# Optimization experiments

Measured on AMD Instinct MI355X. Metric: run time of the kernel, lower is better.

Reference implementation:

```python
import jax, jax.numpy as jnp
import numpy as np

N_NODES = 50000
N_EDGES = 200000
IN_C = 128
HID_C = 128
HEADS = 4
OUT_C = 64
NEG_SLOPE = 0.2


def _glorot(key, shape):
    fan_in, fan_out = shape[0], shape[-1]
    limit = np.sqrt(6.0 / (fan_in + fan_out)).astype(np.float32)
    return jax.random.uniform(key, shape, jnp.float32, -limit, limit)


def setup_inputs() -> dict:
    key = jax.random.key(0)
    ks = jax.random.split(key, 32)
    inp = {}
    inp["x"] = jax.random.normal(ks[0], (N_NODES, IN_C), jnp.float32)
    inp["edge_index"] = jax.random.randint(ks[1], (2, N_EDGES), 0, N_NODES, jnp.int64)
    # layer dims: (in_dim, per_head_out, heads)
    dims = [
        (IN_C, HID_C, HEADS),
        (HID_C * HEADS, HID_C, HEADS),
        (HID_C * HEADS, HID_C, HEADS),
        (HID_C * HEADS, OUT_C, 1),
    ]
    concat = [True, True, True, False]
    kidx = 2
    for i, (din, dout, h) in enumerate(dims):
        inp[f"Wl{i}"] = _glorot(ks[kidx], (din, h * dout)); kidx += 1
        inp[f"bl{i}"] = jnp.zeros((h * dout,), jnp.float32)
        inp[f"Wr{i}"] = _glorot(ks[kidx], (din, h * dout)); kidx += 1
        inp[f"br{i}"] = jnp.zeros((h * dout,), jnp.float32)
        inp[f"att{i}"] = _glorot(ks[kidx], (h, dout)); kidx += 1
        inp[f"b{i}"] = jnp.zeros((h * dout if concat[i] else dout,), jnp.float32)
    return inp


def _segment_softmax(e, seg, num_segments):
    # e: [E, H], seg: [E] target-node ids
    m = jax.ops.segment_max(e, seg, num_segments=num_segments)  # [N, H]
    ex = jnp.exp(e - m[seg])
    s = jax.ops.segment_sum(ex, seg, num_segments=num_segments)  # [N, H]
    return ex / (s[seg] + 1e-16)


def _gatv2_layer(x, src, dst, Wl, bl, Wr, br, att, bias, heads, out_c, concat):
    n = x.shape[0]
    xl = (x @ Wl + bl).reshape(n, heads, out_c)  # source transform
    xr = (x @ Wr + br).reshape(n, heads, out_c)  # target transform
    # GATv2 attention: e_ij = a^T LeakyReLU(xl_j + xr_i)
    z = jax.nn.leaky_relu(xl[src] + xr[dst], NEG_SLOPE)  # [E, H, C]
    e = jnp.einsum("ehc,hc->eh", z, att)  # [E, H]
    alpha = _segment_softmax(e, dst, n)  # [E, H]
    out = jax.ops.segment_sum(alpha[:, :, None] * xl[src], dst, num_segments=n)  # [N, H, C]
    out = out.reshape(n, heads * out_c) if concat else out.mean(axis=1)
    return out + bias


def reference(x, edge_index,
              Wl0, bl0, Wr0, br0, att0, b0,
              Wl1, bl1, Wr1, br1, att1, b1,
              Wl2, bl2, Wr2, br2, att2, b2,
              Wl3, bl3, Wr3, br3, att3, b3):
    src, dst = edge_index[0], edge_index[1]
    layers = [
        (Wl0, bl0, Wr0, br0, att0, b0, HEADS, HID_C, True),
        (Wl1, bl1, Wr1, br1, att1, b1, HEADS, HID_C, True),
        (Wl2, bl2, Wr2, br2, att2, b2, HEADS, HID_C, True),
    ]
    h = x
    for (Wl, bl, Wr, br, att, b, nh, dc, cc) in layers:
        h = jax.nn.elu(_gatv2_layer(h, src, dst, Wl, bl, Wr, br, att, b, nh, dc, cc))
    out = _gatv2_layer(h, src, dst, Wl3, bl3, Wr3, br3, att3, b3, 1, OUT_C, False)
    return out
```

## Files before the change

### kernel.cpp

```cpp
#include <hip/hip_runtime.h>
#include <math.h>

#define NNODES 50000
#define NEDGES 200000

typedef unsigned short ushort_t;
using frag8 = __attribute__((ext_vector_type(8))) short;
using facc4 = __attribute__((ext_vector_type(4))) float;

static __device__ __forceinline__ ushort_t f2b(float f) {
  union { float f; unsigned u; } v; v.f = f;
  unsigned r = v.u + 0x7FFFu + ((v.u >> 16) & 1u);
  return (ushort_t)(r >> 16);
}
static __device__ __forceinline__ float b2f(unsigned hi) {
  return __uint_as_float(hi << 16);
}
static __device__ __forceinline__ void unpack8(const int4 v, float* f) {
  f[0] = b2f((unsigned)v.x & 0xFFFFu); f[1] = b2f((unsigned)v.x >> 16);
  f[2] = b2f((unsigned)v.y & 0xFFFFu); f[3] = b2f((unsigned)v.y >> 16);
  f[4] = b2f((unsigned)v.z & 0xFFFFu); f[5] = b2f((unsigned)v.z >> 16);
  f[6] = b2f((unsigned)v.w & 0xFFFFu); f[7] = b2f((unsigned)v.w >> 16);
}
static __device__ __forceinline__ void stf(float* p, float v) { *p = v; }
static __device__ __forceinline__ void stf(ushort_t* p, float v) { *p = f2b(v); }

__global__ void cast_x(const float* __restrict__ x, ushort_t* __restrict__ xb, int total8) {
  int t = blockIdx.x * 256 + threadIdx.x;
  if (t >= total8) return;
  const float4* p = (const float4*)(x + (size_t)t * 8);
  float4 a = p[0], b = p[1];
  int4 w = make_int4(
      (int)((unsigned)f2b(a.x) | ((unsigned)f2b(a.y) << 16)),
      (int)((unsigned)f2b(a.z) | ((unsigned)f2b(a.w) << 16)),
      (int)((unsigned)f2b(b.x) | ((unsigned)f2b(b.y) << 16)),
      (int)((unsigned)f2b(b.z) | ((unsigned)f2b(b.w) << 16)));
  *(int4*)(xb + (size_t)t * 8) = w;
}

__global__ void wt_prep2(const float* __restrict__ Wl, const float* __restrict__ Wr,
                         ushort_t* __restrict__ WtLR, int K, int Mo) {
  int t = blockIdx.x * 256 + threadIdx.x;
  const int tot = K * Mo;
  if (t >= 2 * tot) return;
  const float* W = (t < tot) ? Wl : Wr;
  int u = (t < tot) ? t : t - tot;
  int c = u / K, k = u - c * K;
  WtLR[t] = f2b(W[(size_t)k * Mo + c]);
}

__global__ __launch_bounds__(256) void gemm2_mfma(
    const ushort_t* __restrict__ A, const ushort_t* __restrict__ WtLR,
    const float* __restrict__ bl, const float* __restrict__ br,
    ushort_t* __restrict__ xlb, ushort_t* __restrict__ xrb,
    int N, int K, int Mo, int ncb) {
  __shared__ __align__(16) char smem[34816];
  auto Al = reinterpret_cast<ushort_t(*)[128][8]>(smem);
  auto Bl = reinterpret_cast<ushort_t(*)[128][8]>(smem + 8192);
  auto Cl = reinterpret_cast<ushort_t(*)[136]>(smem);

  const int nwg = gridDim.x;
  const int q = nwg >> 3, r = nwg & 7;
  const int xcd = blockIdx.x & 7, pos = blockIdx.x >> 3;
  const int orig = (xcd < r ? xcd * (q + 1) : r * (q + 1) + (xcd - r) * q) + pos;
  const int rp = orig / ncb, cb = orig - rp * ncb;
  const int brow = rp * 128;
  const int bcol = cb * 128;

  const int tid = threadIdx.x;
  const int wave = tid >> 6, lane = tid & 63;
  const int wr = wave >> 1, wc = wave & 1;
  const int l15 = lane & 15, l4 = lane >> 4;

  facc4 acc[4][4] = {};

  const int srow = tid >> 1;
  const int skb  = (tid & 1) * 2;
  for (int k0 = 0; k0 < K; k0 += 32) {
    {
      const int grow = brow + srow;
      int4 a0, a1;
      if (grow < N) {
        const int4* pa = (const int4*)(A + (size_t)grow * K + k0 + skb * 8);
        a0 = pa[0]; a1 = pa[1];
      } else {
        a0 = a1 = make_int4(0, 0, 0, 0);
      }
      *(int4*)&Al[skb + 0][srow][0] = a0;
      *(int4*)&Al[skb + 1][srow][0] = a1;
      const int4* pb = (const int4*)(WtLR + (size_t)(bcol + srow) * K + k0 + skb * 8);
      int4 b0 = pb[0], b1 = pb[1];
      *(int4*)&Bl[skb + 0][srow][0] = b0;
      *(int4*)&Bl[skb + 1][srow][0] = b1;
    }
    __syncthreads();
    frag8 af[4], bfg[4];
    #pragma unroll
    for (int i = 0; i < 4; ++i)
      af[i] = *(const frag8*)&Al[l4][wr * 64 + i * 16 + l15][0];
    #pragma unroll
    for (int j = 0; j < 4; ++j)
      bfg[j] = *(const frag8*)&Bl[l4][wc * 64 + j * 16 + l15][0];
    #pragma unroll
    for (int i = 0; i < 4; ++i)
      #pragma unroll
      for (int j = 0; j < 4; ++j)
        acc[i][j] = __builtin_amdgcn_mfma_f32_16x16x32_bf16(af[i], bfg[j], acc[i][j], 0, 0, 0);
    __syncthreads();
  }

  #pragma unroll
  for (int j = 0; j < 4; ++j) {
    const int lcol = wc * 64 + j * 16 + l15;
    const int col2 = bcol + lcol;
    const float bv = (col2 < Mo) ? bl[col2] : br[col2 - Mo];
    #pragma unroll
    for (int i = 0; i < 4; ++i) {
      const int lrow = wr * 64 + i * 16 + l4 * 4;
      #pragma unroll
      for (int rr = 0; rr < 4; ++rr)
        Cl[lrow + rr][lcol] = f2b(acc[i][j][rr] + bv);
    }
  }
  __syncthreads();
  {
    const int row = tid >> 1;
    const int half = tid & 1;
    const int grow = brow + row;
    if (grow < N) {
      const int colb = half * 64;
      const int col2 = bcol + colb;
      const bool isL = col2 < Mo;
      ushort_t* dst = (isL ? xlb : xrb) + (size_t)grow * Mo + (isL ? col2 : col2 - Mo);
      #pragma unroll
      for (int k = 0; k < 8; ++k) {
        int4 v = *(const int4*)&Cl[row][colb + k * 8];
        *(int4*)(dst + k * 8) = v;
      }
    }
  }
}

__global__ void csr_zero(int* __restrict__ deg) {
  int t = blockIdx.x * blockDim.x + threadIdx.x;
  if (t < NNODES) deg[t] = 0;
}
__global__ void csr_hist(const int* __restrict__ ei, int* __restrict__ deg) {
  int e = blockIdx.x * blockDim.x + threadIdx.x;
  if (e >= NEDGES) return;
  atomicAdd(&deg[ei[NEDGES + e]], 1);
}

#define SCAN_TPB 256
#define SCAN_EPT 4
#define SCAN_CHUNK (SCAN_TPB * SCAN_EPT)
#define SCAN_BLK ((NNODES + SCAN_CHUNK - 1) / SCAN_CHUNK)

__global__ __launch_bounds__(SCAN_TPB) void scan_k1(const int* __restrict__ deg,
                                                    int* __restrict__ bsum) {
  __shared__ int sd[SCAN_TPB];
  const int tid = threadIdx.x;
  const int tbase = blockIdx.x * SCAN_CHUNK + tid * SCAN_EPT;
  int s = 0;
  #pragma unroll
  for (int j = 0; j < SCAN_EPT; ++j) {
    int idx = tbase + j;
    if (idx < NNODES) s += deg[idx];
  }
  sd[tid] = s;
  __syncthreads();
  for (int d = SCAN_TPB / 2; d > 0; d >>= 1) {
    if (tid < d) sd[tid] += sd[tid + d];
    __syncthreads();
  }
  if (tid == 0) bsum[blockIdx.x] = sd[0];
}

__global__ __launch_bounds__(64) void scan_k2(const int* __restrict__ bsum,
                                              int* __restrict__ bpref,
                                              int* __restrict__ off) {
  __shared__ int sd[64];
  const int tid = threadIdx.x;
  sd[tid] = (tid < SCAN_BLK) ? bsum[tid] : 0;
  __syncthreads();
  for (int d = 1; d < 64; d <<= 1) {
    int t = (tid >= d) ? sd[tid - d] : 0;
    __syncthreads();
    sd[tid] += t;
    __syncthreads();
  }
  if (tid < SCAN_BLK) bpref[tid] = (tid == 0) ? 0 : sd[tid - 1];
  if (tid == 0) off[NNODES] = NEDGES;
}

__global__ __launch_bounds__(SCAN_TPB) void scan_k3(const int* __restrict__ deg,
                                                    const int* __restrict__ bpref,
                                                    int* __restrict__ off,
                                                    int* __restrict__ pos) {
  __shared__ int sd[SCAN_TPB];
  const int tid = threadIdx.x;
  const int tbase = blockIdx.x * SCAN_CHUNK + tid * SCAN_EPT;
  int v[SCAN_EPT];
  int s = 0;
  #pragma unroll
  for (int j = 0; j < SCAN_EPT; ++j) {
    int idx = tbase + j;
    v[j] = (idx < NNODES) ? deg[idx] : 0;
    s += v[j];
  }
  sd[tid] = s;
  __syncthreads();
  for (int d = 1; d < SCAN_TPB; d <<= 1) {
    int t = (tid >= d) ? sd[tid - d] : 0;
    __syncthreads();
    sd[tid] += t;
    __syncthreads();
  }
  int run = bpref[blockIdx.x] + ((tid == 0) ? 0 : sd[tid - 1]);
  #pragma unroll
  for (int j = 0; j < SCAN_EPT; ++j) {
    int idx = tbase + j;
    if (idx < NNODES) { off[idx] = run; pos[idx] = run; run += v[j]; }
  }
}

__global__ void csr_fill(const int* __restrict__ ei, int* __restrict__ pos,
                         int* __restrict__ eids) {
  int e = blockIdx.x * blockDim.x + threadIdx.x;
  if (e >= NEDGES) return;
  int p = atomicAdd(&pos[ei[NEDGES + e]], 1);
  eids[p] = e;
}

template<int H, int C, bool ELU, typename TO>
__global__ __launch_bounds__(256) void csr_fused(
    const int* __restrict__ off, const int* __restrict__ eids,
    const int* __restrict__ ei, const ushort_t* __restrict__ xl,
    const ushort_t* __restrict__ xr, const float* __restrict__ att,
    const float* __restrict__ bias, TO* __restrict__ out) {
  constexpr int HC = H * C;
  constexpr int CPL = HC / 64;
  constexpr int GROUP = C / CPL;
  const int n = (blockIdx.x * blockDim.x + threadIdx.x) >> 6;
  const int lane = threadIdx.x & 63;
  if (n >= NNODES) return;
  const int s0 = off[n], s1 = off[n + 1];

  float xrr[CPL], atr[CPL];
  if constexpr (CPL == 8) {
    unpack8(*(const int4*)(xr + (size_t)n * HC + lane * 8), xrr);
    const float4 a0 = *(const float4*)(att + lane * 8);
    const float4 a1 = *(const float4*)(att + lane * 8 + 4);
    atr[0] = a0.x; atr[1] = a0.y; atr[2] = a0.z; atr[3] = a0.w;
    atr[4] = a1.x; atr[5] = a1.y; atr[6] = a1.z; atr[7] = a1.w;
  } else {
    xrr[0] = b2f(xr[(size_t)n * HC + lane]);
    atr[0] = att[lane];
  }

  float m = -1e30f, s = 0.f;
  float acc[CPL] = {};

  int4 vnext = make_int4(0, 0, 0, 0);
  ushort_t unext = 0;
  if (s0 < s1) {
    const int srcn = ei[eids[s0]];
    if constexpr (CPL == 8) vnext = *(const int4*)(xl + (size_t)srcn * HC + lane * 8);
    else                    unext = xl[(size_t)srcn * HC + lane];
  }
  for (int i = s0; i < s1; ++i) {
    int4 vcur = vnext; ushort_t ucur = unext;
    if (i + 1 < s1) {
      const int srcn = ei[eids[i + 1]];
      if constexpr (CPL == 8) vnext = *(const int4*)(xl + (size_t)srcn * HC + lane * 8);
      else                    unext = xl[(size_t)srcn * HC + lane];
    }
    float zl[CPL];
    if constexpr (CPL == 8) unpack8(vcur, zl);
    else zl[0] = b2f(ucur);
    float e = 0.f;
    #pragma unroll
    for (int c = 0; c < CPL; ++c) {
      float z = zl[c] + xrr[c];
      z = (z > 0.f) ? z : 0.2f * z;
      e += z * atr[c];
    }
    #pragma unroll
    for (int o = 1; o < GROUP; o <<= 1)
      e += __shfl_xor(e, o, 64);
    if (e > m) {
      const float scale = __expf(m - e);
      s *= scale;
      #pragma unroll
      for (int c = 0; c < CPL; ++c) acc[c] *= scale;
      m = e;
    }
    const float w = __expf(e - m);
    s += w;
    #pragma unroll
    for (int c = 0; c < CPL; ++c) acc[c] += w * zl[c];
  }
  const float inv = 1.f / (s + 1e-16f);
  TO* po = out + (size_t)n * HC + lane * CPL;
  #pragma unroll
  for (int c = 0; c < CPL; ++c) {
    float v = acc[c] * inv + bias[lane * CPL + c];
    if (ELU) v = v > 0.f ? v : (__expf(v) - 1.f);
    stf(&po[c], v);
  }
}

__global__ void report_ws(float* __restrict__ out, float v) { out[0] = v; }

extern "C" void kernel_launch(void* const* d_in, const int* in_sizes, int n_in,
                              void* d_out, int out_size, void* d_ws, size_t ws_size,
                              hipStream_t stream) {
  const float* x  = (const float*)d_in[0];
  const int*   ei = (const int*)d_in[1];
  float* out = (float*)d_out;
  char* ws = (char*)d_ws;

  ushort_t* hbuf = (ushort_t*)(ws);
  ushort_t* xlb  = (ushort_t*)(ws + 51200000ull);
  ushort_t* xrb  = (ushort_t*)(ws + 102400000ull);
  ushort_t* xb   = (ushort_t*)(ws + 153600000ull);
  ushort_t* WtLR = (ushort_t*)(ws + 166400000ull);
  int* bsum  = (int*)(ws + 168500000ull);
  int* bpref = (int*)(ws + 168501024ull);
  int* coff  = (int*)(ws + 168600000ull);
  int* cpos  = (int*)(ws + 168800008ull);
  int* cdeg  = (int*)(ws + 169000012ull);
  int* eids  = (int*)(ws + 169200016ull);

  if (ws_size < 170000016ull) {
    report_ws<<<1, 1, 0, stream>>>(out, (float)ws_size);
    return;
  }

  cast_x<<<(NNODES * 128 / 8 + 255) / 256, 256, 0, stream>>>(x, xb, NNODES * 128 / 8);
  csr_zero<<<(NNODES + 255) / 256, 256, 0, stream>>>(cdeg);
  csr_hist<<<(NEDGES + 255) / 256, 256, 0, stream>>>(ei, cdeg);
  scan_k1<<<SCAN_BLK, SCAN_TPB, 0, stream>>>(cdeg, bsum);
  scan_k2<<<1, 64, 0, stream>>>(bsum, bpref, coff);
  scan_k3<<<SCAN_BLK, SCAN_TPB, 0, stream>>>(cdeg, bpref, coff, cpos);
  csr_fill<<<(NEDGES + 255) / 256, 256, 0, stream>>>(ei, cpos, eids);

  const int ngrid = (NNODES * 64 + 255) / 256;
  const int nrp = (NNODES + 127) / 128;

  for (int layer = 0; layer < 4; ++layer) {
    const int base = 2 + layer * 6;
    const float* Wl  = (const float*)d_in[base + 0];
    const float* bl  = (const float*)d_in[base + 1];
    const float* Wr  = (const float*)d_in[base + 2];
    const float* br  = (const float*)d_in[base + 3];
    const float* att = (const float*)d_in[base + 4];
    const float* b   = (const float*)d_in[base + 5];

    const ushort_t* A = (layer == 0) ? xb : hbuf;
    const int K  = (layer == 0) ? 128 : 512;
    const int Mo = (layer == 3) ? 64 : 512;
    const int ncb = 2 * Mo / 128;

    wt_prep2<<<(2 * K * Mo + 255) / 256, 256, 0, stream>>>(Wl, Wr, WtLR, K, Mo);

    gemm2_mfma<<<ncb * nrp, 256, 0, stream>>>(A, WtLR, bl, br, xlb, xrb,
                                              NNODES, K, Mo, ncb);

    if (layer < 3) {
      csr_fused<4, 128, true, ushort_t><<<ngrid, 256, 0, stream>>>(
          coff, eids, ei, xlb, xrb, att, b, hbuf);
    } else {
      csr_fused<1, 64, false, float><<<ngrid, 256, 0, stream>>>(
          coff, eids, ei, xlb, xrb, att, b, out);
    }
  }
}
```

Measured before the change: 528.9 us.

## Prefetch GEMM tiles with BK=64, tile-transpose weights, store source ids in CSR

The GEMM now uses a K-step of 64 and register-prefetches the next A/B tile while MFMAs run on the current one, halving barrier count per K. Weight transpose/cast uses a 32x32 shared-memory tile for coalesced reads and writes instead of strided per-element loads. The CSR fill stores source node ids directly so the aggregation kernel drops one dependent indirection, and the next source id is prefetched two edges ahead. More registers are used in the GEMM, which may reduce occupancy.

```diff
diff --git a/kernel.cpp b/kernel.cpp
--- a/kernel.cpp
+++ b/kernel.cpp
@@ -38,25 +38,34 @@
   *(int4*)(xb + (size_t)t * 8) = w;
 }
 
-__global__ void wt_prep2(const float* __restrict__ Wl, const float* __restrict__ Wr,
-                         ushort_t* __restrict__ WtLR, int K, int Mo) {
-  int t = blockIdx.x * 256 + threadIdx.x;
-  const int tot = K * Mo;
-  if (t >= 2 * tot) return;
-  const float* W = (t < tot) ? Wl : Wr;
-  int u = (t < tot) ? t : t - tot;
-  int c = u / K, k = u - c * K;
-  WtLR[t] = f2b(W[(size_t)k * Mo + c]);
-}
-
-__global__ __launch_bounds__(256) void gemm2_mfma(
+__global__ __launch_bounds__(256) void wt_prep_t(
+    const float* __restrict__ Wl, const float* __restrict__ Wr,
+    ushort_t* __restrict__ WtLR, int K, int Mo) {
+  __shared__ float tile[32][33];
+  const int tx = threadIdx.x & 31, ty = threadIdx.x >> 5;
+  const int kb = blockIdx.y * 32, cb = blockIdx.x * 32;
+  const int c2 = cb + tx;
+  const float* W = (c2 < Mo) ? Wl : Wr;
+  const int col = (c2 < Mo) ? c2 : c2 - Mo;
+  #pragma unroll
+  for (int r = 0; r < 4; ++r)
+    tile[ty * 4 + r][tx] = W[(size_t)(kb + ty * 4 + r) * Mo + col];
+  __syncthreads();
+  #pragma unroll
+  for (int r = 0; r < 4; ++r) {
+    const int c2w = cb + ty * 4 + r;
+    WtLR[(size_t)c2w * K + kb + tx] = f2b(tile[tx][ty * 4 + r]);
+  }
+}
+
+__global__ __launch_bounds__(256) void gemm2_pf64(
     const ushort_t* __restrict__ A, const ushort_t* __restrict__ WtLR,
     const float* __restrict__ bl, const float* __restrict__ br,
     ushort_t* __restrict__ xlb, ushort_t* __restrict__ xrb,
     int N, int K, int Mo, int ncb) {
   __shared__ __align__(16) char smem[34816];
   auto Al = reinterpret_cast<ushort_t(*)[128][8]>(smem);
-  auto Bl = reinterpret_cast<ushort_t(*)[128][8]>(smem + 8192);
+  auto Bl = reinterpret_cast<ushort_t(*)[128][8]>(smem + 16384);
   auto Cl = reinterpret_cast<ushort_t(*)[136]>(smem);
 
   const int nwg = gridDim.x;
@@ -68,44 +77,62 @@
   const int bcol = cb * 128;
 
   const int tid = threadIdx.x;
-  const int wave = tid >> 6, lane = tid & 63;
-  const int wr = wave >> 1, wc = wave & 1;
+  const int w = tid >> 6, lane = tid & 63;
+  const int wr = w >> 1, wc = w & 1;
   const int l15 = lane & 15, l4 = lane >> 4;
 
   facc4 acc[4][4] = {};
 
   const int srow = tid >> 1;
-  const int skb  = (tid & 1) * 2;
-  for (int k0 = 0; k0 < K; k0 += 32) {
-    {
-      const int grow = brow + srow;
-      int4 a0, a1;
-      if (grow < N) {
-        const int4* pa = (const int4*)(A + (size_t)grow * K + k0 + skb * 8);
-        a0 = pa[0]; a1 = pa[1];
-      } else {
-        a0 = a1 = make_int4(0, 0, 0, 0);
+  const int sk4  = (tid & 1) * 4;
+  const int grow = brow + srow;
+  const bool rowok = grow < N;
+  const ushort_t* pa = A + (size_t)(rowok ? grow : 0) * K + sk4 * 8;
+  const ushort_t* pb = WtLR + (size_t)(bcol + srow) * K + sk4 * 8;
+
+  const int nt = K >> 6;
+
+  int4 ar[4], br_[4];
+  if (rowok) {
+    const int4* p = (const int4*)pa;
+    ar[0] = p[0]; ar[1] = p[1]; ar[2] = p[2]; ar[3] = p[3];
+  } else {
+    ar[0] = ar[1] = ar[2] = ar[3] = make_int4(0, 0, 0, 0);
+  }
+  { const int4* p = (const int4*)pb;
+    br_[0] = p[0]; br_[1] = p[1]; br_[2] = p[2]; br_[3] = p[3]; }
+
+  for (int t = 0; t < nt; ++t) {
+    #pragma unroll
+    for (int j = 0; j < 4; ++j) {
+      *(int4*)&Al[sk4 + j][srow][0] = ar[j];
+      *(int4*)&Bl[sk4 + j][srow][0] = br_[j];
+    }
+    if (t + 1 < nt) {
+      const int k0 = (t + 1) * 64;
+      if (rowok) {
+        const int4* p = (const int4*)(pa + k0);
+        ar[0] = p[0]; ar[1] = p[1]; ar[2] = p[2]; ar[3] = p[3];
       }
-      *(int4*)&Al[skb + 0][srow][0] = a0;
-      *(int4*)&Al[skb + 1][srow][0] = a1;
-      const int4* pb = (const int4*)(WtLR + (size_t)(bcol + srow) * K + k0 + skb * 8);
-      int4 b0 = pb[0], b1 = pb[1];
-      *(int4*)&Bl[skb + 0][srow][0] = b0;
-      *(int4*)&Bl[skb + 1][srow][0] = b1;
-    }
-    __syncthreads();
-    frag8 af[4], bfg[4];
-    #pragma unroll
-    for (int i = 0; i < 4; ++i)
-      af[i] = *(const frag8*)&Al[l4][wr * 64 + i * 16 + l15][0];
-    #pragma unroll
-    for (int j = 0; j < 4; ++j)
-      bfg[j] = *(const frag8*)&Bl[l4][wc * 64 + j * 16 + l15][0];
-    #pragma unroll
-    for (int i = 0; i < 4; ++i)
+      { const int4* p = (const int4*)(pb + k0);
+        br_[0] = p[0]; br_[1] = p[1]; br_[2] = p[2]; br_[3] = p[3]; }
+    }
+    __syncthreads();
+    #pragma unroll
+    for (int kk = 0; kk < 2; ++kk) {
+      frag8 af[4], bfg[4];
+      #pragma unroll
+      for (int i = 0; i < 4; ++i)
+        af[i] = *(const frag8*)&Al[kk * 4 + l4][wr * 64 + i * 16 + l15][0];
       #pragma unroll
       for (int j = 0; j < 4; ++j)
-        acc[i][j] = __builtin_amdgcn_mfma_f32_16x16x32_bf16(af[i], bfg[j], acc[i][j], 0, 0, 0);
+        bfg[j] = *(const frag8*)&Bl[kk * 4 + l4][wc * 64 + j * 16 + l15][0];
+      #pragma unroll
+      for (int i = 0; i < 4; ++i)
+        #pragma unroll
+        for (int j = 0; j < 4; ++j)
+          acc[i][j] = __builtin_amdgcn_mfma_f32_16x16x32_bf16(af[i], bfg[j], acc[i][j], 0, 0, 0);
+    }
     __syncthreads();
   }
 
@@ -126,12 +153,12 @@
   {
     const int row = tid >> 1;
     const int half = tid & 1;
-    const int grow = brow + row;
-    if (grow < N) {
+    const int growo = brow + row;
+    if (growo < N) {
       const int colb = half * 64;
       const int col2 = bcol + colb;
       const bool isL = col2 < Mo;
-      ushort_t* dst = (isL ? xlb : xrb) + (size_t)grow * Mo + (isL ? col2 : col2 - Mo);
+      ushort_t* dst = (isL ? xlb : xrb) + (size_t)growo * Mo + (isL ? col2 : col2 - Mo);
       #pragma unroll
       for (int k = 0; k < 8; ++k) {
         int4 v = *(const int4*)&Cl[row][colb + k * 8];
@@ -225,19 +252,19 @@
 }
 
 __global__ void csr_fill(const int* __restrict__ ei, int* __restrict__ pos,
-                         int* __restrict__ eids) {
+                         int* __restrict__ srcs) {
   int e = blockIdx.x * blockDim.x + threadIdx.x;
   if (e >= NEDGES) return;
   int p = atomicAdd(&pos[ei[NEDGES + e]], 1);
-  eids[p] = e;
+  srcs[p] = ei[e];
 }
 
 template<int H, int C, bool ELU, typename TO>
 __global__ __launch_bounds__(256) void csr_fused(
-    const int* __restrict__ off, const int* __restrict__ eids,
-    const int* __restrict__ ei, const ushort_t* __restrict__ xl,
-    const ushort_t* __restrict__ xr, const float* __restrict__ att,
-    const float* __restrict__ bias, TO* __restrict__ out) {
+    const int* __restrict__ off, const int* __restrict__ srcs,
+    const ushort_t* __restrict__ xl, const ushort_t* __restrict__ xr,
+    const float* __restrict__ att, const float* __restrict__ bias,
+    TO* __restrict__ out) {
   constexpr int HC = H * C;
   constexpr int CPL = HC / 64;
   constexpr int GROUP = C / CPL;
@@ -263,17 +290,20 @@
 
   int4 vnext = make_int4(0, 0, 0, 0);
   ushort_t unext = 0;
+  int snext = 0;
   if (s0 < s1) {
-    const int srcn = ei[eids[s0]];
+    const int srcn = srcs[s0];
     if constexpr (CPL == 8) vnext = *(const int4*)(xl + (size_t)srcn * HC + lane * 8);
     else                    unext = xl[(size_t)srcn * HC + lane];
+    if (s0 + 1 < s1) snext = srcs[s0 + 1];
   }
   for (int i = s0; i < s1; ++i) {
     int4 vcur = vnext; ushort_t ucur = unext;
+    const int sn = snext;
+    if (i + 2 < s1) snext = srcs[i + 2];
     if (i + 1 < s1) {
-      const int srcn = ei[eids[i + 1]];
-      if constexpr (CPL == 8) vnext = *(const int4*)(xl + (size_t)srcn * HC + lane * 8);
-      else                    unext = xl[(size_t)srcn * HC + lane];
+      if constexpr (CPL == 8) vnext = *(const int4*)(xl + (size_t)sn * HC + lane * 8);
+      else                    unext = xl[(size_t)sn * HC + lane];
     }
     float zl[CPL];
     if constexpr (CPL == 8) unpack8(vcur, zl);
@@ -330,7 +360,7 @@
   int* coff  = (int*)(ws + 168600000ull);
   int* cpos  = (int*)(ws + 168800008ull);
   int* cdeg  = (int*)(ws + 169000012ull);
-  int* eids  = (int*)(ws + 169200016ull);
+  int* srcs  = (int*)(ws + 169200016ull);
 
   if (ws_size < 170000016ull) {
     report_ws<<<1, 1, 0, stream>>>(out, (float)ws_size);
@@ -343,7 +373,7 @@
   scan_k1<<<SCAN_BLK, SCAN_TPB, 0, stream>>>(cdeg, bsum);
   scan_k2<<<1, 64, 0, stream>>>(bsum, bpref, coff);
   scan_k3<<<SCAN_BLK, SCAN_TPB, 0, stream>>>(cdeg, bpref, coff, cpos);
-  csr_fill<<<(NEDGES + 255) / 256, 256, 0, stream>>>(ei, cpos, eids);
+  csr_fill<<<(NEDGES + 255) / 256, 256, 0, stream>>>(ei, cpos, srcs);
 
   const int ngrid = (NNODES * 64 + 255) / 256;
   const int nrp = (NNODES + 127) / 128;
@@ -362,17 +392,18 @@
     const int Mo = (layer == 3) ? 64 : 512;
     const int ncb = 2 * Mo / 128;
 
-    wt_prep2<<<(2 * K * Mo + 255) / 256, 256, 0, stream>>>(Wl, Wr, WtLR, K, Mo);
-
-    gemm2_mfma<<<ncb * nrp, 256, 0, stream>>>(A, WtLR, bl, br, xlb, xrb,
+    dim3 wg(2 * Mo / 32, K / 32);
+    wt_prep_t<<<wg, 256, 0, stream>>>(Wl, Wr, WtLR, K, Mo);
+
+    gemm2_pf64<<<ncb * nrp, 256, 0, stream>>>(A, WtLR, bl, br, xlb, xrb,
                                               NNODES, K, Mo, ncb);
 
     if (layer < 3) {
       csr_fused<4, 128, true, ushort_t><<<ngrid, 256, 0, stream>>>(
-          coff, eids, ei, xlb, xrb, att, b, hbuf);
+          coff, srcs, xlb, xrb, att, b, hbuf);
     } else {
       csr_fused<1, 64, false, float><<<ngrid, 256, 0, stream>>>(
-          coff, eids, ei, xlb, xrb, att, b, out);
-    }
-  }
-}
+          coff, srcs, xlb, xrb, att, b, out);
+    }
+  }
+}
```

New measurement: 623.5 us. +17.9%, slower.
